# Optimization experiments

Hardware: AMD Instinct MI355X
Metric: run time of the kernel (lower is better)

The kernel has to match this reference:

```python
import jax, jax.numpy as jnp
import numpy as np

HEAD_DIM = 64
N_HEADS = 32
N_KV_HEADS = 8
ROPE_THETA = 10000.0
NEG_INF = -1e9


def _rope_cos_sin(position_ids, head_dim, dtype):
    # position_ids: [b, s] int -> cos/sin [b, s, head_dim]
    inv_freq = 1.0 / (ROPE_THETA ** (jnp.arange(0, head_dim, 2, dtype=jnp.float32) / head_dim))
    freqs = position_ids.astype(jnp.float32)[..., None] * inv_freq  # [b, s, d/2]
    emb = jnp.concatenate([freqs, freqs], axis=-1)                  # [b, s, d]
    return jnp.cos(emb).astype(dtype), jnp.sin(emb).astype(dtype)


def _rotate_half(x):
    half = x.shape[-1] // 2
    return jnp.concatenate([-x[..., half:], x[..., :half]], axis=-1)


def setup_inputs() -> dict:
    key = jax.random.key(0)
    ks = jax.random.split(key, 6)
    b, s, din = 2, 2048, 4096  # din = 2 * hidden_size
    hidden_states = jax.random.normal(ks[0], (b, s, din), dtype=jnp.float32)
    # additive causal mask [b, 1, q, kv]
    causal = jnp.tril(jnp.ones((s, s), dtype=bool))
    attention_mask = jnp.where(causal, 0.0, NEG_INF).astype(jnp.float32)
    attention_mask = jnp.broadcast_to(attention_mask[None, None], (b, 1, s, s))
    position_ids = jnp.broadcast_to(jnp.arange(s, dtype=jnp.int32)[None], (b, s))
    scale = 0.02
    Wq = jax.random.normal(ks[1], (din, N_HEADS * HEAD_DIM), dtype=jnp.float32) * scale
    Wk = jax.random.normal(ks[2], (din, N_KV_HEADS * HEAD_DIM), dtype=jnp.float32) * scale
    Wv = jax.random.normal(ks[3], (din, N_KV_HEADS * HEAD_DIM), dtype=jnp.float32) * scale
    Wo = jax.random.normal(ks[4], (N_HEADS * HEAD_DIM, din // 2), dtype=jnp.float32) * scale
    return {"hidden_states": hidden_states, "attention_mask": attention_mask,
            "position_ids": position_ids, "Wq": Wq, "Wk": Wk, "Wv": Wv, "Wo": Wo}


def reference(hidden_states, attention_mask, position_ids, Wq, Wk, Wv, Wo):
    b, s, _ = hidden_states.shape
    g = N_HEADS // N_KV_HEADS  # GQA group size
    q = (hidden_states @ Wq).reshape(b, s, N_HEADS, HEAD_DIM).transpose(0, 2, 1, 3)      # [b,h,s,d]
    k = (hidden_states @ Wk).reshape(b, s, N_KV_HEADS, HEAD_DIM).transpose(0, 2, 1, 3)   # [b,kh,s,d]
    v = (hidden_states @ Wv).reshape(b, s, N_KV_HEADS, HEAD_DIM).transpose(0, 2, 1, 3)
    cos, sin = _rope_cos_sin(position_ids, HEAD_DIM, q.dtype)  # [b,s,d]
    cos, sin = cos[:, None], sin[:, None]                      # [b,1,s,d]
    q = q * cos + _rotate_half(q) * sin
    k = k * cos + _rotate_half(k) * sin
    # GQA: group query heads instead of materializing repeated K/V
    qg = q.reshape(b, N_KV_HEADS, g, s, HEAD_DIM)
    scores = jnp.einsum('bhgqd,bhkd->bhgqk', qg, k) / jnp.sqrt(jnp.float32(HEAD_DIM))
    scores = scores + attention_mask[:, :, None]               # broadcast over kv-head, group
    probs = jax.nn.softmax(scores.astype(jnp.float32), axis=-1).astype(q.dtype)
    out = jnp.einsum('bhgqk,bhkd->bhgqd', probs, v)            # [b,kh,g,s,d]
    out = out.reshape(b, N_HEADS, s, HEAD_DIM).transpose(0, 2, 1, 3).reshape(b, s, N_HEADS * HEAD_DIM)
    return out @ Wo
```

## Files before the change

kernel.cpp:

```cpp
#include <hip/hip_runtime.h>
#include <hip/hip_bf16.h>
#include <cstdint>
#include <cstddef>

typedef __attribute__((ext_vector_type(4))) float floatx4;
typedef __attribute__((ext_vector_type(8))) short shortx8;

typedef __attribute__((address_space(1))) void gvoid;
typedef __attribute__((address_space(3))) void lvoid;

__device__ inline __hip_bfloat16 f2b(float x) { return __float2bfloat16(x); }
__device__ inline float b2f(__hip_bfloat16 x) { return __bfloat162float(x); }
__device__ inline unsigned short f2bu(float x) {
  __hip_bfloat16 h = __float2bfloat16(x);
  return *reinterpret_cast<unsigned short*>(&h);
}

template <typename T> __device__ inline T cvt_out(float x);
template <> __device__ inline float cvt_out<float>(float x) { return x; }
template <> __device__ inline __hip_bfloat16 cvt_out<__hip_bfloat16>(float x) { return __float2bfloat16(x); }

__global__ void cvt_f32_bf16(const float* __restrict__ in, __hip_bfloat16* __restrict__ out, int n) {
  int i = (blockIdx.x * blockDim.x + threadIdx.x) * 4;
  if (i >= n) return;
  float4 v = *(const float4*)(in + i);
  __hip_bfloat16 o[4] = { f2b(v.x), f2b(v.y), f2b(v.z), f2b(v.w) };
  *(ushort4*)(out + i) = *(const ushort4*)o;
}

__global__ void transpose_cvt(const float* __restrict__ in, __hip_bfloat16* __restrict__ out, int K, int N) {
  __shared__ float tile[32][33];
  int n0 = blockIdx.x * 32, k0 = blockIdx.y * 32;
  int tx = threadIdx.x, ty = threadIdx.y;
#pragma unroll
  for (int i = 0; i < 4; i++)
    tile[ty + i * 8][tx] = in[(size_t)(k0 + ty + i * 8) * N + n0 + tx];
  __syncthreads();
#pragma unroll
  for (int i = 0; i < 4; i++)
    out[(size_t)(n0 + ty + i * 8) * K + k0 + tx] = f2b(tile[tx][ty + i * 8]);
}

template <typename OutT>
__global__ __launch_bounds__(256) void gemm_bt(
    const __hip_bfloat16* __restrict__ A,
    const __hip_bfloat16* __restrict__ Bt,
    OutT* __restrict__ C, int M, int N, int K) {
  __shared__ short lA[128 * 32];
  __shared__ short lB[128 * 32];
  const int m0 = blockIdx.x * 128, n0 = blockIdx.y * 128;
  const int t = threadIdx.x;
  const int l = t & 63;
  const int w = t >> 6;
  const int wm = (w & 1) * 64, wn = (w >> 1) * 64;
  const int lr = l & 15, lq = l >> 4;
  floatx4 acc[4][4] = {};

  for (int kt = 0; kt < K; kt += 32) {
    __syncthreads();
#pragma unroll
    for (int j = 0; j < 2; j++) {
      int flat = j * 2048 + t * 8;
      const __hip_bfloat16* srcA = A + (size_t)(m0 + (flat >> 5)) * K + kt + (flat & 31);
      __builtin_amdgcn_global_load_lds((gvoid*)srcA, (lvoid*)&lA[flat], 16, 0, 0);
      const __hip_bfloat16* srcB = Bt + (size_t)(n0 + (flat >> 5)) * K + kt + (flat & 31);
      __builtin_amdgcn_global_load_lds((gvoid*)srcB, (lvoid*)&lB[flat], 16, 0, 0);
    }
    __syncthreads();
    shortx8 af[4], bfr[4];
#pragma unroll
    for (int mi = 0; mi < 4; mi++)
      af[mi] = *(const shortx8*)&lA[(wm + mi * 16 + lr) * 32 + lq * 8];
#pragma unroll
    for (int ni = 0; ni < 4; ni++)
      bfr[ni] = *(const shortx8*)&lB[(wn + ni * 16 + lr) * 32 + lq * 8];
#pragma unroll
    for (int mi = 0; mi < 4; mi++)
#pragma unroll
      for (int ni = 0; ni < 4; ni++)
        acc[mi][ni] = __builtin_amdgcn_mfma_f32_16x16x32_bf16(af[mi], bfr[ni], acc[mi][ni], 0, 0, 0);
  }
#pragma unroll
  for (int mi = 0; mi < 4; mi++)
#pragma unroll
    for (int ni = 0; ni < 4; ni++) {
      int row = m0 + wm + mi * 16 + lq * 4;
      int col = n0 + wn + ni * 16 + lr;
#pragma unroll
      for (int r = 0; r < 4; r++)
        C[(size_t)(row + r) * N + col] = cvt_out<OutT>(acc[mi][ni][r]);
    }
}

__global__ void rope_kernel(__hip_bfloat16* __restrict__ q, int stride, float scale) {
  int i = threadIdx.x;
  int row = blockIdx.x * 8 + threadIdx.y;
  int head = blockIdx.y;
  int pos = row & 2047;
  float freq = (float)pos * exp2f(-(float)i * (13.287712379549449f / 32.0f));
  float s = sinf(freq), c = cosf(freq);
  __hip_bfloat16* p = q + (size_t)row * stride + head * 64 + i;
  float x1 = b2f(p[0]), x2 = b2f(p[32]);
  p[0]  = f2b((x1 * c - x2 * s) * scale);
  p[32] = f2b((x2 * c + x1 * s) * scale);
}

__global__ void v_transpose(const __hip_bfloat16* __restrict__ QKV, __hip_bfloat16* __restrict__ Vt) {
  __shared__ __hip_bfloat16 tile[32][33];
  int bkvh = blockIdx.z;
  int s0 = blockIdx.x * 32, d0 = blockIdx.y * 32;
  int b = bkvh >> 3, kvh = bkvh & 7;
  int tx = threadIdx.x, ty = threadIdx.y;
#pragma unroll
  for (int i = 0; i < 4; i++)
    tile[ty + i * 8][tx] = QKV[(size_t)(b * 2048 + s0 + ty + i * 8) * 3072 + 2560 + kvh * 64 + d0 + tx];
  __syncthreads();
#pragma unroll
  for (int i = 0; i < 4; i++)
    Vt[((size_t)(bkvh * 64 + d0 + ty + i * 8) << 11) + s0 + tx] = tile[tx][ty + i * 8];
}

__global__ __launch_bounds__(256, 3) void attn_kernel(
    const __hip_bfloat16* __restrict__ Qp,
    const __hip_bfloat16* __restrict__ Kp,
    const __hip_bfloat16* __restrict__ Vt,
    __hip_bfloat16* __restrict__ O) {
  __shared__ __align__(16) short lK[2][64 * 64];
  __shared__ __align__(16) short lV[2][64 * 64];
  __shared__ __align__(16) short lP[4][16 * 64];
  const int h = blockIdx.y, b = blockIdx.z;
  const int ia = ((int)blockIdx.x + (h & 15) + ((h >> 4) << 3) + (b << 2)) & 15;
  const int ib = 31 - ia;
  const int kvh = h >> 2;
  const int t = threadIdx.x, w = t >> 6, l = t & 63;
  const int lr = l & 15, lq = l >> 4;
  const int swz = lr & 7;

  const int q0A = ia * 64 + w * 16;
  const int q0B = ib * 64 + w * 16;
  const __hip_bfloat16* qpA = Qp + (size_t)(b * 2048 + q0A + lr) * 3072 + h * 64 + lq * 8;
  const __hip_bfloat16* qpB = Qp + (size_t)(b * 2048 + q0B + lr) * 3072 + h * 64 + lq * 8;
  shortx8 qfA0 = *(const shortx8*)(qpA);
  shortx8 qfA1 = *(const shortx8*)(qpA + 32);
  shortx8 qfB0 = *(const shortx8*)(qpB);
  shortx8 qfB1 = *(const shortx8*)(qpB + 32);

  const int srow = t >> 3, schunk = t & 7;
  const __hip_bfloat16* ksrc = Kp + (size_t)(b * 2048 + srow) * 3072 + kvh * 64 + schunk * 8;
  const __hip_bfloat16* vsrc = Vt + ((size_t)((b * 8 + kvh) * 64 + srow) << 11) + schunk * 8;
  const int ldst = srow * 64 + ((schunk ^ (srow & 7)) << 3);
  short* const myP = &lP[w][0];

  floatx4 oA[4] = {}, oB[4] = {};
  float mA = -1e30f, sumA = 0.f, mB = -1e30f, sumB = 0.f;

  uint4 kreg[2], vreg[2];
  const int KT = 32 - ia;
#pragma unroll
  for (int j = 0; j < 2; j++) {
    kreg[j] = *(const uint4*)(ksrc + (size_t)(j * 32) * 3072);
    vreg[j] = *(const uint4*)(vsrc + (size_t)(j * 32) * 2048);
  }

  for (int kt = 0; kt < KT; kt++) {
    const int buf = kt & 1;
#pragma unroll
    for (int j = 0; j < 2; j++) {
      *(uint4*)&lK[buf][ldst + j * 2048] = kreg[j];
      *(uint4*)&lV[buf][ldst + j * 2048] = vreg[j];
    }
    __syncthreads();
    if (kt + 1 < KT) {
#pragma unroll
      for (int j = 0; j < 2; j++) {
        kreg[j] = *(const uint4*)(ksrc + (size_t)((kt + 1) * 64 + j * 32) * 3072);
        vreg[j] = *(const uint4*)(vsrc + (size_t)(j * 32) * 2048 + (kt + 1) * 64);
      }
    }
    const bool doA = (kt <= ia);

    floatx4 sA[4] = {}, sB[4] = {};
    __builtin_amdgcn_s_setprio(1);
#pragma unroll
    for (int mi = 0; mi < 4; mi++) {
      const short* kr = &lK[buf][(mi * 16 + lr) * 64];
      shortx8 kf0 = *(const shortx8*)(kr + ((lq ^ swz) << 3));
      shortx8 kf1 = *(const shortx8*)(kr + (((4 + lq) ^ swz) << 3));
      if (doA) {
        sA[mi] = __builtin_amdgcn_mfma_f32_16x16x32_bf16(kf0, qfA0, sA[mi], 0, 0, 0);
        sA[mi] = __builtin_amdgcn_mfma_f32_16x16x32_bf16(kf1, qfA1, sA[mi], 0, 0, 0);
      }
      sB[mi] = __builtin_amdgcn_mfma_f32_16x16x32_bf16(kf0, qfB0, sB[mi], 0, 0, 0);
      sB[mi] = __builtin_amdgcn_mfma_f32_16x16x32_bf16(kf1, qfB1, sB[mi], 0, 0, 0);
    }
    __builtin_amdgcn_s_setprio(0);

    shortx8 pA0, pA1, pB0, pB1;
    float alphaA = 1.f, alphaB = 1.f;
    bool rescA = false, rescB = false;

    if (doA) {
      if (kt == ia) {
#pragma unroll
        for (int mi = 0; mi < 4; mi++)
#pragma unroll
          for (int r = 0; r < 4; r++)
            if (mi * 16 + lq * 4 + r > w * 16 + lr) sA[mi][r] = -3e8f;
      }
      float mx = sA[0][0];
#pragma unroll
      for (int mi = 0; mi < 4; mi++)
#pragma unroll
        for (int r = 0; r < 4; r++) mx = fmaxf(mx, sA[mi][r]);
      mx = fmaxf(mx, __shfl_xor(mx, 16, 64));
      mx = fmaxf(mx, __shfl_xor(mx, 32, 64));
      rescA = !__all(mx <= mA + 8.f);
      if (rescA) {
        float mnew = fmaxf(mA, mx);
        alphaA = exp2f(mA - mnew);
        mA = mnew;
      }
      float rs = 0.f;
#pragma unroll
      for (int mi = 0; mi < 4; mi++)
#pragma unroll
        for (int r = 0; r < 4; r++) {
          float pv = exp2f(sA[mi][r] - mA);
          sA[mi][r] = pv;
          rs += pv;
        }
      rs += __shfl_xor(rs, 16, 64);
      rs += __shfl_xor(rs, 32, 64);
      sumA = rescA ? sumA * alphaA + rs : sumA + rs;
#pragma unroll
      for (int mi = 0; mi < 4; mi++) {
        uint2 val;
        val.x = (unsigned)f2bu(sA[mi][0]) | ((unsigned)f2bu(sA[mi][1]) << 16);
        val.y = (unsigned)f2bu(sA[mi][2]) | ((unsigned)f2bu(sA[mi][3]) << 16);
        *(uint2*)(myP + lr * 64 + (((mi * 2 + (lq >> 1)) ^ swz) << 3) + ((lq & 1) << 2)) = val;
      }
      pA0 = *(const shortx8*)(myP + lr * 64 + ((lq ^ swz) << 3));
      pA1 = *(const shortx8*)(myP + lr * 64 + (((4 + lq) ^ swz) << 3));
    }

    {
      if (kt == KT - 1) {
#pragma unroll
        for (int mi = 0; mi < 4; mi++)
#pragma unroll
          for (int r = 0; r < 4; r++)
            if (mi * 16 + lq * 4 + r > w * 16 + lr) sB[mi][r] = -3e8f;
      }
      float mx = sB[0][0];
#pragma unroll
      for (int mi = 0; mi < 4; mi++)
#pragma unroll
        for (int r = 0; r < 4; r++) mx = fmaxf(mx, sB[mi][r]);
      mx = fmaxf(mx, __shfl_xor(mx, 16, 64));
      mx = fmaxf(mx, __shfl_xor(mx, 32, 64));
      rescB = !__all(mx <= mB + 8.f);
      if (rescB) {
        float mnew = fmaxf(mB, mx);
        alphaB = exp2f(mB - mnew);
        mB = mnew;
      }
      float rs = 0.f;
#pragma unroll
      for (int mi = 0; mi < 4; mi++)
#pragma unroll
        for (int r = 0; r < 4; r++) {
          float pv = exp2f(sB[mi][r] - mB);
          sB[mi][r] = pv;
          rs += pv;
        }
      rs += __shfl_xor(rs, 16, 64);
      rs += __shfl_xor(rs, 32, 64);
      sumB = rescB ? sumB * alphaB + rs : sumB + rs;
#pragma unroll
      for (int mi = 0; mi < 4; mi++) {
        uint2 val;
        val.x = (unsigned)f2bu(sB[mi][0]) | ((unsigned)f2bu(sB[mi][1]) << 16);
        val.y = (unsigned)f2bu(sB[mi][2]) | ((unsigned)f2bu(sB[mi][3]) << 16);
        *(uint2*)(myP + lr * 64 + (((mi * 2 + (lq >> 1)) ^ swz) << 3) + ((lq & 1) << 2)) = val;
      }
      pB0 = *(const shortx8*)(myP + lr * 64 + ((lq ^ swz) << 3));
      pB1 = *(const shortx8*)(myP + lr * 64 + (((4 + lq) ^ swz) << 3));
    }

    __builtin_amdgcn_s_setprio(1);
#pragma unroll
    for (int mi = 0; mi < 4; mi++) {
      const short* vr = &lV[buf][(mi * 16 + lr) * 64];
      shortx8 vf0 = *(const shortx8*)(vr + ((lq ^ swz) << 3));
      shortx8 vf1 = *(const shortx8*)(vr + (((4 + lq) ^ swz) << 3));
      if (doA) {
        floatx4 o = oA[mi];
        if (rescA) {
#pragma unroll
          for (int r = 0; r < 4; r++) o[r] *= alphaA;
        }
        o = __builtin_amdgcn_mfma_f32_16x16x32_bf16(vf0, pA0, o, 0, 0, 0);
        o = __builtin_amdgcn_mfma_f32_16x16x32_bf16(vf1, pA1, o, 0, 0, 0);
        oA[mi] = o;
      }
      floatx4 o2 = oB[mi];
      if (rescB) {
#pragma unroll
        for (int r = 0; r < 4; r++) o2[r] *= alphaB;
      }
      o2 = __builtin_amdgcn_mfma_f32_16x16x32_bf16(vf0, pB0, o2, 0, 0, 0);
      o2 = __builtin_amdgcn_mfma_f32_16x16x32_bf16(vf1, pB1, o2, 0, 0, 0);
      oB[mi] = o2;
    }
    __builtin_amdgcn_s_setprio(0);
  }

  const float livA = 1.f / sumA, livB = 1.f / sumB;
  __hip_bfloat16* obase = O + (size_t)(b * 2048 + q0A + lr) * 2048 + h * 64 + lq * 4;
#pragma unroll
  for (int mi = 0; mi < 4; mi++) {
    ushort4 pk;
    pk.x = f2bu(oA[mi][0] * livA); pk.y = f2bu(oA[mi][1] * livA);
    pk.z = f2bu(oA[mi][2] * livA); pk.w = f2bu(oA[mi][3] * livA);
    *(ushort4*)(obase + mi * 16) = pk;
  }
  __hip_bfloat16* obase2 = O + (size_t)(b * 2048 + q0B + lr) * 2048 + h * 64 + lq * 4;
#pragma unroll
  for (int mi = 0; mi < 4; mi++) {
    ushort4 pk;
    pk.x = f2bu(oB[mi][0] * livB); pk.y = f2bu(oB[mi][1] * livB);
    pk.z = f2bu(oB[mi][2] * livB); pk.w = f2bu(oB[mi][3] * livB);
    *(ushort4*)(obase2 + mi * 16) = pk;
  }
}

extern "C" void kernel_launch(void* const* d_in, const int* in_sizes, int n_in,
                              void* d_out, int out_size, void* d_ws, size_t ws_size,
                              hipStream_t stream) {
  (void)in_sizes; (void)n_in; (void)out_size; (void)ws_size;
  const float* hs = (const float*)d_in[0];
  const float* Wq = (const float*)d_in[3];
  const float* Wk = (const float*)d_in[4];
  const float* Wv = (const float*)d_in[5];
  const float* Wo = (const float*)d_in[6];
  float* out = (float*)d_out;

  char* p = (char*)d_ws;
  auto alloc = [&](size_t elts) { __hip_bfloat16* r = (__hip_bfloat16*)p; p += elts * 2; return r; };
  __hip_bfloat16* Xb   = alloc(4096ull * 4096);
  __hip_bfloat16* Wt   = alloc(3072ull * 4096);
  __hip_bfloat16* Wot  = alloc(2048ull * 2048);
  __hip_bfloat16* QKVb = alloc(4096ull * 3072);
  __hip_bfloat16* Vtb  = alloc(2ull * 8 * 64 * 2048);
  __hip_bfloat16* Ab   = alloc(4096ull * 2048);

  cvt_f32_bf16<<<16384, 256, 0, stream>>>(hs, Xb, 4096 * 4096);
  transpose_cvt<<<dim3(64, 128), dim3(32, 8), 0, stream>>>(Wq, Wt, 4096, 2048);
  transpose_cvt<<<dim3(16, 128), dim3(32, 8), 0, stream>>>(Wk, Wt + 2048ull * 4096, 4096, 512);
  transpose_cvt<<<dim3(16, 128), dim3(32, 8), 0, stream>>>(Wv, Wt + 2560ull * 4096, 4096, 512);
  transpose_cvt<<<dim3(64, 64), dim3(32, 8), 0, stream>>>(Wo, Wot, 2048, 2048);

  gemm_bt<__hip_bfloat16><<<dim3(32, 24), 256, 0, stream>>>(Xb, Wt, QKVb, 4096, 3072, 4096);

  rope_kernel<<<dim3(512, 32), dim3(32, 8), 0, stream>>>(QKVb, 3072, 0.18033688011112042f);
  rope_kernel<<<dim3(512, 8), dim3(32, 8), 0, stream>>>(QKVb + 2048, 3072, 1.0f);
  v_transpose<<<dim3(64, 2, 16), dim3(32, 8), 0, stream>>>(QKVb, Vtb);

  attn_kernel<<<dim3(16, 32, 2), 256, 0, stream>>>(QKVb, QKVb + 2048, Vtb, Ab);

  gemm_bt<float><<<dim3(32, 16), 256, 0, stream>>>(Ab, Wot, out, 4096, 2048, 2048);
}
```

Baseline: 558.1 us.

## Stage K/V tiles with direct global-to-LDS loads and packed bf16 conversions

The attention kernel now moves K and V tiles straight from global memory into LDS with global_load_lds, applying the swizzle on the source address. This replaces the register round-trip followed by an LDS store. The softmax max and sum reductions become trees to shorten dependency chains, and bf16 packing uses the hardware v_cvt_pk_bf16_f32 instruction. The risk is that the async LDS writes depend on __syncthreads and vmcnt waits for correctness, and the per-wave LDS destination layout has to match the swizzled reads.

Measured after the change: 557.9 us. No clear change (-0.0%).

```diff
diff --git a/kernel.cpp b/kernel.cpp
--- a/kernel.cpp
+++ b/kernel.cpp
@@ -14,6 +14,11 @@
 __device__ inline unsigned short f2bu(float x) {
   __hip_bfloat16 h = __float2bfloat16(x);
   return *reinterpret_cast<unsigned short*>(&h);
+}
+__device__ inline unsigned cvt_pk_bf16(float lo, float hi) {
+  unsigned r;
+  asm("v_cvt_pk_bf16_f32 %0, %1, %2" : "=v"(r) : "v"(lo), "v"(hi));
+  return r;
 }
 
 template <typename T> __device__ inline T cvt_out(float x);
@@ -146,37 +151,32 @@
   shortx8 qfB1 = *(const shortx8*)(qpB + 32);
 
   const int srow = t >> 3, schunk = t & 7;
-  const __hip_bfloat16* ksrc = Kp + (size_t)(b * 2048 + srow) * 3072 + kvh * 64 + schunk * 8;
-  const __hip_bfloat16* vsrc = Vt + ((size_t)((b * 8 + kvh) * 64 + srow) << 11) + schunk * 8;
-  const int ldst = srow * 64 + ((schunk ^ (srow & 7)) << 3);
+  const int swzch = schunk ^ (srow & 7);
+  const __hip_bfloat16* ksrc = Kp + (size_t)(b * 2048 + srow) * 3072 + kvh * 64 + swzch * 8;
+  const __hip_bfloat16* vsrc = Vt + ((size_t)((b * 8 + kvh) * 64 + srow) << 11) + swzch * 8;
   short* const myP = &lP[w][0];
 
   floatx4 oA[4] = {}, oB[4] = {};
   float mA = -1e30f, sumA = 0.f, mB = -1e30f, sumB = 0.f;
 
-  uint4 kreg[2], vreg[2];
   const int KT = 32 - ia;
-#pragma unroll
-  for (int j = 0; j < 2; j++) {
-    kreg[j] = *(const uint4*)(ksrc + (size_t)(j * 32) * 3072);
-    vreg[j] = *(const uint4*)(vsrc + (size_t)(j * 32) * 2048);
-  }
+
+  auto stage = [&](int sbuf, int kt2) {
+#pragma unroll
+    for (int j = 0; j < 2; j++) {
+      __builtin_amdgcn_global_load_lds((gvoid*)(ksrc + (size_t)(kt2 * 64 + j * 32) * 3072),
+                                       (lvoid*)&lK[sbuf][w * 512 + j * 2048], 16, 0, 0);
+      __builtin_amdgcn_global_load_lds((gvoid*)(vsrc + (size_t)(j * 32) * 2048 + kt2 * 64),
+                                       (lvoid*)&lV[sbuf][w * 512 + j * 2048], 16, 0, 0);
+    }
+  };
+
+  stage(0, 0);
 
   for (int kt = 0; kt < KT; kt++) {
     const int buf = kt & 1;
-#pragma unroll
-    for (int j = 0; j < 2; j++) {
-      *(uint4*)&lK[buf][ldst + j * 2048] = kreg[j];
-      *(uint4*)&lV[buf][ldst + j * 2048] = vreg[j];
-    }
     __syncthreads();
-    if (kt + 1 < KT) {
-#pragma unroll
-      for (int j = 0; j < 2; j++) {
-        kreg[j] = *(const uint4*)(ksrc + (size_t)((kt + 1) * 64 + j * 32) * 3072);
-        vreg[j] = *(const uint4*)(vsrc + (size_t)(j * 32) * 2048 + (kt + 1) * 64);
-      }
-    }
+    if (kt + 1 < KT) stage(buf ^ 1, kt + 1);
     const bool doA = (kt <= ia);
 
     floatx4 sA[4] = {}, sB[4] = {};
@@ -207,11 +207,11 @@
           for (int r = 0; r < 4; r++)
             if (mi * 16 + lq * 4 + r > w * 16 + lr) sA[mi][r] = -3e8f;
       }
-      float mx = sA[0][0];
+      float pm[4];
 #pragma unroll
       for (int mi = 0; mi < 4; mi++)
-#pragma unroll
-        for (int r = 0; r < 4; r++) mx = fmaxf(mx, sA[mi][r]);
+        pm[mi] = fmaxf(fmaxf(sA[mi][0], sA[mi][1]), fmaxf(sA[mi][2], sA[mi][3]));
+      float mx = fmaxf(fmaxf(pm[0], pm[1]), fmaxf(pm[2], pm[3]));
       mx = fmaxf(mx, __shfl_xor(mx, 16, 64));
       mx = fmaxf(mx, __shfl_xor(mx, 32, 64));
       rescA = !__all(mx <= mA + 8.f);
@@ -220,23 +220,23 @@
         alphaA = exp2f(mA - mnew);
         mA = mnew;
       }
-      float rs = 0.f;
-#pragma unroll
-      for (int mi = 0; mi < 4; mi++)
-#pragma unroll
-        for (int r = 0; r < 4; r++) {
-          float pv = exp2f(sA[mi][r] - mA);
-          sA[mi][r] = pv;
-          rs += pv;
-        }
+      float rsm[4];
+#pragma unroll
+      for (int mi = 0; mi < 4; mi++) {
+        float p0 = exp2f(sA[mi][0] - mA), p1 = exp2f(sA[mi][1] - mA);
+        float p2 = exp2f(sA[mi][2] - mA), p3 = exp2f(sA[mi][3] - mA);
+        sA[mi][0] = p0; sA[mi][1] = p1; sA[mi][2] = p2; sA[mi][3] = p3;
+        rsm[mi] = (p0 + p1) + (p2 + p3);
+      }
+      float rs = (rsm[0] + rsm[1]) + (rsm[2] + rsm[3]);
       rs += __shfl_xor(rs, 16, 64);
       rs += __shfl_xor(rs, 32, 64);
       sumA = rescA ? sumA * alphaA + rs : sumA + rs;
 #pragma unroll
       for (int mi = 0; mi < 4; mi++) {
         uint2 val;
-        val.x = (unsigned)f2bu(sA[mi][0]) | ((unsigned)f2bu(sA[mi][1]) << 16);
-        val.y = (unsigned)f2bu(sA[mi][2]) | ((unsigned)f2bu(sA[mi][3]) << 16);
+        val.x = cvt_pk_bf16(sA[mi][0], sA[mi][1]);
+        val.y = cvt_pk_bf16(sA[mi][2], sA[mi][3]);
         *(uint2*)(myP + lr * 64 + (((mi * 2 + (lq >> 1)) ^ swz) << 3) + ((lq & 1) << 2)) = val;
       }
       pA0 = *(const shortx8*)(myP + lr * 64 + ((lq ^ swz) << 3));
@@ -251,11 +251,11 @@
           for (int r = 0; r < 4; r++)
             if (mi * 16 + lq * 4 + r > w * 16 + lr) sB[mi][r] = -3e8f;
       }
-      float mx = sB[0][0];
+      float pm[4];
 #pragma unroll
       for (int mi = 0; mi < 4; mi++)
-#pragma unroll
-        for (int r = 0; r < 4; r++) mx = fmaxf(mx, sB[mi][r]);
+        pm[mi] = fmaxf(fmaxf(sB[mi][0], sB[mi][1]), fmaxf(sB[mi][2], sB[mi][3]));
+      float mx = fmaxf(fmaxf(pm[0], pm[1]), fmaxf(pm[2], pm[3]));
       mx = fmaxf(mx, __shfl_xor(mx, 16, 64));
       mx = fmaxf(mx, __shfl_xor(mx, 32, 64));
       rescB = !__all(mx <= mB + 8.f);
@@ -264,23 +264,23 @@
         alphaB = exp2f(mB - mnew);
         mB = mnew;
       }
-      float rs = 0.f;
-#pragma unroll
-      for (int mi = 0; mi < 4; mi++)
-#pragma unroll
-        for (int r = 0; r < 4; r++) {
-          float pv = exp2f(sB[mi][r] - mB);
-          sB[mi][r] = pv;
-          rs += pv;
-        }
+      float rsm[4];
+#pragma unroll
+      for (int mi = 0; mi < 4; mi++) {
+        float p0 = exp2f(sB[mi][0] - mB), p1 = exp2f(sB[mi][1] - mB);
+        float p2 = exp2f(sB[mi][2] - mB), p3 = exp2f(sB[mi][3] - mB);
+        sB[mi][0] = p0; sB[mi][1] = p1; sB[mi][2] = p2; sB[mi][3] = p3;
+        rsm[mi] = (p0 + p1) + (p2 + p3);
+      }
+      float rs = (rsm[0] + rsm[1]) + (rsm[2] + rsm[3]);
       rs += __shfl_xor(rs, 16, 64);
       rs += __shfl_xor(rs, 32, 64);
       sumB = rescB ? sumB * alphaB + rs : sumB + rs;
 #pragma unroll
       for (int mi = 0; mi < 4; mi++) {
         uint2 val;
-        val.x = (unsigned)f2bu(sB[mi][0]) | ((unsigned)f2bu(sB[mi][1]) << 16);
-        val.y = (unsigned)f2bu(sB[mi][2]) | ((unsigned)f2bu(sB[mi][3]) << 16);
+        val.x = cvt_pk_bf16(sB[mi][0], sB[mi][1]);
+        val.y = cvt_pk_bf16(sB[mi][2], sB[mi][3]);
         *(uint2*)(myP + lr * 64 + (((mi * 2 + (lq >> 1)) ^ swz) << 3) + ((lq & 1) << 2)) = val;
       }
       pB0 = *(const shortx8*)(myP + lr * 64 + ((lq ^ swz) << 3));
@@ -319,18 +319,18 @@
   __hip_bfloat16* obase = O + (size_t)(b * 2048 + q0A + lr) * 2048 + h * 64 + lq * 4;
 #pragma unroll
   for (int mi = 0; mi < 4; mi++) {
-    ushort4 pk;
-    pk.x = f2bu(oA[mi][0] * livA); pk.y = f2bu(oA[mi][1] * livA);
-    pk.z = f2bu(oA[mi][2] * livA); pk.w = f2bu(oA[mi][3] * livA);
-    *(ushort4*)(obase + mi * 16) = pk;
+    uint2 pk;
+    pk.x = cvt_pk_bf16(oA[mi][0] * livA, oA[mi][1] * livA);
+    pk.y = cvt_pk_bf16(oA[mi][2] * livA, oA[mi][3] * livA);
+    *(uint2*)(obase + mi * 16) = pk;
   }
   __hip_bfloat16* obase2 = O + (size_t)(b * 2048 + q0B + lr) * 2048 + h * 64 + lq * 4;
 #pragma unroll
   for (int mi = 0; mi < 4; mi++) {
-    ushort4 pk;
-    pk.x = f2bu(oB[mi][0] * livB); pk.y = f2bu(oB[mi][1] * livB);
-    pk.z = f2bu(oB[mi][2] * livB); pk.w = f2bu(oB[mi][3] * livB);
-    *(ushort4*)(obase2 + mi * 16) = pk;
+    uint2 pk;
+    pk.x = cvt_pk_bf16(oB[mi][0] * livB, oB[mi][1] * livB);
+    pk.y = cvt_pk_bf16(oB[mi][2] * livB, oB[mi][3] * livB);
+    *(uint2*)(obase2 + mi * 16) = pk;
   }
 }
 
```
